# Kernel optimization log

Measured on AMD Instinct MI355X. Metric: run time of the kernel, lower is better.

Reference implementation:

```python
import jax, jax.numpy as jnp
import numpy as np

CODEBOOK_SIZE = 4096
DIM = 64


def setup_inputs() -> dict:
    key = jax.random.key(0)
    kx, ke = jax.random.split(key)
    x = jax.random.normal(kx, (8, 4096, DIM), dtype=jnp.float32)
    embed = jax.random.normal(ke, (CODEBOOK_SIZE, DIM), dtype=jnp.float32)  # codebook [K, d]
    return {"x": x, "embed": embed}


def reference(x, embed):
    # Eval-mode forward of EuclideanCodebook (svq_temp=None -> argmax).
    shape = x.shape
    flatten = x.reshape(-1, shape[-1])            # [N, d]
    embed_sq = jnp.sum(embed * embed, axis=-1)    # [K]
    # dist = 2 * x @ embed.T - ||embed||^2  (negative squared distance up to a const in x)
    dist = 2.0 * jnp.matmul(flatten, embed.T) - embed_sq[None, :]  # [N, K]
    embed_ind = jnp.argmax(dist, axis=-1)         # [N]
    embed_ind = embed_ind.reshape(shape[:-1])     # [...]
    quantize = embed[embed_ind]                   # gather -> [..., d]
    return (quantize, embed_ind)
```

## Files before the change

### kernel.cpp

```cpp
#include <hip/hip_runtime.h>
#include <math.h>

#define N_ROWS 32768
#define K_CODES 4096
#define DIM 64
#define SPLITS 4
#define TILES_TOTAL (K_CODES / 32)
#define TILES_PER_SPLIT (TILES_TOTAL / SPLITS)
#define QUANT_ELEMS (N_ROWS * DIM)

typedef _Float16 half8 __attribute__((ext_vector_type(8)));
typedef float floatx16 __attribute__((ext_vector_type(16)));

#define MFMA32(a, b, c) __builtin_amdgcn_mfma_f32_32x32x16_f16((a), (b), (c), 0, 0, 0)

__device__ __forceinline__ void gld16(const void* g, void* l) {
    __builtin_amdgcn_global_load_lds(
        (const __attribute__((address_space(1))) unsigned int*)g,
        (__attribute__((address_space(3))) unsigned int*)l, 16, 0, 0);
}

__global__ void prep_kernel(const float* __restrict__ embed,
                            float* __restrict__ sq, half8* __restrict__ ehi,
                            half8* __restrict__ elo) {
    __shared__ float part[256];
    const int tid = threadIdx.x;
    const int t = blockIdx.x * 256 + tid;
    const int l = t & 63;
    const int s = (t >> 6) & 3;
    const int c = blockIdx.x;
    const int col = l & 31;
    const int code = c * 32 + col;
    const int koff = (l >> 5) * 8 + 16 * s;
    const float* src = embed + (size_t)code * DIM + koff;
    half8 h, lo;
    float ss = 0.f;
#pragma unroll
    for (int j = 0; j < 8; ++j) {
        float v = src[j];
        ss = fmaf(v, v, ss);
        _Float16 hi = (_Float16)v;
        h[j] = hi;
        lo[j] = (_Float16)(v - (float)hi);
    }
    ehi[t] = h;
    elo[t] = lo;
    part[tid] = ss;
    __syncthreads();
    if (tid < 32) {
        float a = 0.f;
#pragma unroll
        for (int q = 0; q < 8; ++q)
            a += part[tid + 32 * (q & 1) + 64 * (q >> 1)];
        sq[c * 32 + tid] = a;
    }
}

__global__ __launch_bounds__(256, 4) void fused_dist_argmax32(
    const float* __restrict__ x, const float* __restrict__ sq,
    const half8* __restrict__ ehi, const half8* __restrict__ elo,
    float* __restrict__ pbest, int* __restrict__ pidx) {
    __shared__ char lbuf[2][8192];
    const int tid = threadIdx.x;
    const int lane = tid & 63;
    const int wave = tid >> 6;
    const int col = lane & 31;
    const int half_ = lane >> 5;
    const int row_base = blockIdx.x * 128 + wave * 32;
    const int split = blockIdx.y;
    const int c0 = split * TILES_PER_SPLIT;

    half8 ah[4], al[4];
    {
        const float* xs = x + (size_t)(row_base + col) * DIM + half_ * 8;
#pragma unroll
        for (int s = 0; s < 4; ++s) {
            half8 h, lo;
#pragma unroll
            for (int j = 0; j < 8; ++j) {
                float v = 2.0f * xs[16 * s + j];
                _Float16 hi = (_Float16)v;
                h[j] = hi;
                lo[j] = (_Float16)(v - (float)hi);
            }
            ah[s] = h;
            al[s] = lo;
        }
    }

    float best[16];
    int bidx[16];
#pragma unroll
    for (int r = 0; r < 16; ++r) {
        best[r] = -INFINITY;
        bidx[r] = 0;
    }

    const char* gh = (const char*)(ehi + (size_t)c0 * 256);
    const char* gl = (const char*)(elo + (size_t)c0 * 256);
    const float* psq = sq + c0 * 32 + col;

    gld16(gh + (size_t)tid * 16, lbuf[0] + tid * 16);
    gld16(gl + (size_t)tid * 16, lbuf[0] + 4096 + tid * 16);
    __syncthreads();

    for (int c = 0; c < TILES_PER_SPLIT; ++c) {
        const int cur = c & 1;
        const half8* lh = (const half8*)(lbuf[cur]);
        const half8* ll = (const half8*)(lbuf[cur] + 4096);

        half8 bh0 = lh[lane], bh1 = lh[64 + lane], bh2 = lh[128 + lane],
              bh3 = lh[192 + lane];
        half8 bl0 = ll[lane], bl1 = ll[64 + lane], bl2 = ll[128 + lane],
              bl3 = ll[192 + lane];
        float nsq = -psq[(size_t)c * 32];

        if (c + 1 < TILES_PER_SPLIT) {
            const size_t off = (size_t)(c + 1) * 4096 + (size_t)tid * 16;
            gld16(gh + off, lbuf[cur ^ 1] + tid * 16);
            gld16(gl + off, lbuf[cur ^ 1] + 4096 + tid * 16);
        }

        floatx16 acc;
#pragma unroll
        for (int r = 0; r < 16; ++r) acc[r] = nsq;
        acc = MFMA32(ah[0], bh0, acc);
        acc = MFMA32(al[0], bh0, acc);
        acc = MFMA32(ah[0], bl0, acc);
        acc = MFMA32(ah[1], bh1, acc);
        acc = MFMA32(al[1], bh1, acc);
        acc = MFMA32(ah[1], bl1, acc);
        acc = MFMA32(ah[2], bh2, acc);
        acc = MFMA32(al[2], bh2, acc);
        acc = MFMA32(ah[2], bl2, acc);
        acc = MFMA32(ah[3], bh3, acc);
        acc = MFMA32(al[3], bh3, acc);
        acc = MFMA32(ah[3], bl3, acc);

        const int cidx = (c0 + c) * 32 + col;
#pragma unroll
        for (int r = 0; r < 16; ++r) {
            if (acc[r] > best[r]) {
                best[r] = acc[r];
                bidx[r] = cidx;
            }
        }
        __syncthreads();
    }

#pragma unroll
    for (int r = 0; r < 16; ++r) {
        float bv = best[r];
        int bi = bidx[r];
#pragma unroll
        for (int d = 1; d < 32; d <<= 1) {
            float ov = __shfl_xor(bv, d);
            int oi = __shfl_xor(bi, d);
            if (ov > bv || (ov == bv && oi < bi)) {
                bv = ov;
                bi = oi;
            }
        }
        if (col == 0) {
            const int row = row_base + (r & 3) + 8 * (r >> 2) + 4 * half_;
            pbest[(size_t)split * N_ROWS + row] = bv;
            pidx[(size_t)split * N_ROWS + row] = bi;
        }
    }
}

__global__ void combine_kernel(const float* __restrict__ pbest,
                               const int* __restrict__ pidx,
                               const float* __restrict__ embed,
                               float* __restrict__ out) {
    const int t = blockIdx.x * blockDim.x + threadIdx.x;
    const int row = t >> 4;
    const int q = t & 15;
    if (row >= N_ROWS) return;

    float best = -INFINITY;
    int bi = 0;
#pragma unroll
    for (int s = 0; s < SPLITS; ++s) {
        float b = pbest[(size_t)s * N_ROWS + row];
        int i = pidx[(size_t)s * N_ROWS + row];
        if (b > best) {
            best = b;
            bi = i;
        }
    }

    const float4* e4 = reinterpret_cast<const float4*>(embed);
    float4 v = e4[(size_t)bi * (DIM / 4) + q];
    reinterpret_cast<float4*>(out)[(size_t)row * (DIM / 4) + q] = v;
    if (q == 0) {
        out[(size_t)QUANT_ELEMS + row] = (float)bi;
    }
}

extern "C" void kernel_launch(void* const* d_in, const int* in_sizes, int n_in,
                              void* d_out, int out_size, void* d_ws,
                              size_t ws_size, hipStream_t stream) {
    const float* x = (const float*)d_in[0];
    const float* embed = (const float*)d_in[1];
    float* out = (float*)d_out;

    char* ws = (char*)d_ws;
    float* sq = (float*)ws;
    half8* ehi = (half8*)(ws + 16384);
    half8* elo = (half8*)(ws + 16384 + 524288);
    float* pbest = (float*)(ws + 16384 + 2 * 524288);
    int* pidx = (int*)(ws + 16384 + 2 * 524288 + SPLITS * N_ROWS * 4);

    prep_kernel<<<TILES_TOTAL, 256, 0, stream>>>(embed, sq, ehi, elo);

    dim3 grid(N_ROWS / 128, SPLITS);
    fused_dist_argmax32<<<grid, 256, 0, stream>>>(x, sq, ehi, elo, pbest,
                                                  pidx);

    const int combine_threads = N_ROWS * (DIM / 4);
    combine_kernel<<<(combine_threads + 255) / 256, 256, 0, stream>>>(
        pbest, pidx, embed, out);
}
```

Measured before the change: 127.0 us.

## Process two codebook tiles per iteration with 4-deep LDS buffering and 3 splits

The main loop now computes two 32-code tiles per iteration using two independent accumulators, which halves the number of barriers and gives the MFMA chains more independent work. LDS grows to four tile buffers, so two tiles are prefetched while two are computed. The K dimension is split three ways (44/42/42 tiles) instead of four, and launch bounds drop to 3 blocks per CU. The costs are higher register and LDS use, fewer blocks in the grid, and an uneven split.

```diff
diff --git a/kernel.cpp b/kernel.cpp
--- a/kernel.cpp
+++ b/kernel.cpp
@@ -4,9 +4,8 @@
 #define N_ROWS 32768
 #define K_CODES 4096
 #define DIM 64
-#define SPLITS 4
+#define SPLITS 3
 #define TILES_TOTAL (K_CODES / 32)
-#define TILES_PER_SPLIT (TILES_TOTAL / SPLITS)
 #define QUANT_ELEMS (N_ROWS * DIM)
 
 typedef _Float16 half8 __attribute__((ext_vector_type(8)));
@@ -56,11 +55,35 @@
     }
 }
 
-__global__ __launch_bounds__(256, 4) void fused_dist_argmax32(
+#define TILECOMPUTE(A, buf, cc)                                              \
+    {                                                                        \
+        const half8* lh = (const half8*)(buf);                               \
+        const half8* ll = (const half8*)((buf) + 4096);                      \
+        half8 b0 = lh[lane], b1 = lh[64 + lane], b2 = lh[128 + lane],        \
+              b3 = lh[192 + lane];                                           \
+        half8 l0 = ll[lane], l1 = ll[64 + lane], l2 = ll[128 + lane],        \
+              l3 = ll[192 + lane];                                           \
+        float nsq = -psq[(size_t)(cc) * 32];                                 \
+        _Pragma("unroll") for (int r = 0; r < 16; ++r) A[r] = nsq;           \
+        A = MFMA32(ah[0], b0, A);                                            \
+        A = MFMA32(al[0], b0, A);                                            \
+        A = MFMA32(ah[0], l0, A);                                            \
+        A = MFMA32(ah[1], b1, A);                                            \
+        A = MFMA32(al[1], b1, A);                                            \
+        A = MFMA32(ah[1], l1, A);                                            \
+        A = MFMA32(ah[2], b2, A);                                            \
+        A = MFMA32(al[2], b2, A);                                            \
+        A = MFMA32(ah[2], l2, A);                                            \
+        A = MFMA32(ah[3], b3, A);                                            \
+        A = MFMA32(al[3], b3, A);                                            \
+        A = MFMA32(ah[3], l3, A);                                            \
+    }
+
+__global__ __launch_bounds__(256, 3) void fused_dist_argmax32(
     const float* __restrict__ x, const float* __restrict__ sq,
     const half8* __restrict__ ehi, const half8* __restrict__ elo,
     float* __restrict__ pbest, int* __restrict__ pidx) {
-    __shared__ char lbuf[2][8192];
+    __shared__ char lbuf[4][8192];
     const int tid = threadIdx.x;
     const int lane = tid & 63;
     const int wave = tid >> 6;
@@ -68,7 +91,8 @@
     const int half_ = lane >> 5;
     const int row_base = blockIdx.x * 128 + wave * 32;
     const int split = blockIdx.y;
-    const int c0 = split * TILES_PER_SPLIT;
+    const int c0 = (split == 0) ? 0 : ((split == 1) ? 44 : 86);
+    const int nt = (split == 0) ? 44 : 42;
 
     half8 ah[4], al[4];
     {
@@ -100,49 +124,41 @@
     const char* gl = (const char*)(elo + (size_t)c0 * 256);
     const float* psq = sq + c0 * 32 + col;
 
-    gld16(gh + (size_t)tid * 16, lbuf[0] + tid * 16);
-    gld16(gl + (size_t)tid * 16, lbuf[0] + 4096 + tid * 16);
+    {
+        const size_t o = (size_t)tid * 16;
+        gld16(gh + o, lbuf[0] + tid * 16);
+        gld16(gl + o, lbuf[0] + 4096 + tid * 16);
+        gld16(gh + 4096 + o, lbuf[1] + tid * 16);
+        gld16(gl + 4096 + o, lbuf[1] + 4096 + tid * 16);
+    }
     __syncthreads();
 
-    for (int c = 0; c < TILES_PER_SPLIT; ++c) {
-        const int cur = c & 1;
-        const half8* lh = (const half8*)(lbuf[cur]);
-        const half8* ll = (const half8*)(lbuf[cur] + 4096);
-
-        half8 bh0 = lh[lane], bh1 = lh[64 + lane], bh2 = lh[128 + lane],
-              bh3 = lh[192 + lane];
-        half8 bl0 = ll[lane], bl1 = ll[64 + lane], bl2 = ll[128 + lane],
-              bl3 = ll[192 + lane];
-        float nsq = -psq[(size_t)c * 32];
-
-        if (c + 1 < TILES_PER_SPLIT) {
-            const size_t off = (size_t)(c + 1) * 4096 + (size_t)tid * 16;
-            gld16(gh + off, lbuf[cur ^ 1] + tid * 16);
-            gld16(gl + off, lbuf[cur ^ 1] + 4096 + tid * 16);
-        }
-
-        floatx16 acc;
-#pragma unroll
-        for (int r = 0; r < 16; ++r) acc[r] = nsq;
-        acc = MFMA32(ah[0], bh0, acc);
-        acc = MFMA32(al[0], bh0, acc);
-        acc = MFMA32(ah[0], bl0, acc);
-        acc = MFMA32(ah[1], bh1, acc);
-        acc = MFMA32(al[1], bh1, acc);
-        acc = MFMA32(ah[1], bl1, acc);
-        acc = MFMA32(ah[2], bh2, acc);
-        acc = MFMA32(al[2], bh2, acc);
-        acc = MFMA32(ah[2], bl2, acc);
-        acc = MFMA32(ah[3], bh3, acc);
-        acc = MFMA32(al[3], bh3, acc);
-        acc = MFMA32(ah[3], bl3, acc);
-
-        const int cidx = (c0 + c) * 32 + col;
+    for (int c = 0; c < nt; c += 2) {
+        if (c + 2 < nt) {
+            const size_t o2 = (size_t)(c + 2) * 4096 + (size_t)tid * 16;
+            char* d2 = lbuf[(c + 2) & 3];
+            gld16(gh + o2, d2 + tid * 16);
+            gld16(gl + o2, d2 + 4096 + tid * 16);
+            const size_t o3 = o2 + 4096;
+            char* d3 = lbuf[(c + 3) & 3];
+            gld16(gh + o3, d3 + tid * 16);
+            gld16(gl + o3, d3 + 4096 + tid * 16);
+        }
+
+        floatx16 acc0, acc1;
+        TILECOMPUTE(acc0, lbuf[c & 3], c)
+        TILECOMPUTE(acc1, lbuf[(c + 1) & 3], c + 1)
+
+        const int cidx0 = (c0 + c) * 32 + col;
 #pragma unroll
         for (int r = 0; r < 16; ++r) {
-            if (acc[r] > best[r]) {
-                best[r] = acc[r];
-                bidx[r] = cidx;
+            if (acc0[r] > best[r]) {
+                best[r] = acc0[r];
+                bidx[r] = cidx0;
+            }
+            if (acc1[r] > best[r]) {
+                best[r] = acc1[r];
+                bidx[r] = cidx0 + 32;
             }
         }
         __syncthreads();
```

Result: faster. 123.7 us (-2.6%).
